# Optimization experiments

Hardware: AMD Instinct MI355X
Metric: run time of the kernel (lower is better)

## Reference

```python
import jax, jax.numpy as jnp
import numpy as np

N_NODES = 100000


def gcn_conv(x, W, b, edge_index, n_nodes):
    # PyG GCNConv (default args): add self-loops, symmetric normalization,
    # linear transform first, then normalized scatter-add aggregation, then bias.
    h = x @ W  # [N, out]
    loop = jnp.arange(n_nodes, dtype=edge_index.dtype)
    row = jnp.concatenate([edge_index[0], loop])  # sources
    col = jnp.concatenate([edge_index[1], loop])  # targets
    deg = jax.ops.segment_sum(jnp.ones_like(col, dtype=h.dtype), col, num_segments=n_nodes)
    dinv = jnp.where(deg > 0, jax.lax.rsqrt(deg), 0.0)
    norm = dinv[row] * dinv[col]  # [E']
    msg = h[row] * norm[:, None]  # gather + scale
    out = jax.ops.segment_sum(msg, col, num_segments=n_nodes)  # scatter-add
    return out + b


def setup_inputs() -> dict:
    key = jax.random.key(0)
    k1, k2, k3, k4 = jax.random.split(key, 4)
    N, E, F, H, C = N_NODES, 3200000, 128, 16, 8
    x = jax.random.normal(k1, (N, F), dtype=jnp.float32)
    edge_index = jax.random.randint(k2, (2, E), 0, N, dtype=jnp.int64)
    W1 = jax.random.normal(k3, (F, H), dtype=jnp.float32) / np.sqrt(F)
    b1 = jnp.zeros((H,), dtype=jnp.float32)
    W2 = jax.random.normal(k4, (H, C), dtype=jnp.float32) / np.sqrt(H)
    b2 = jnp.zeros((C,), dtype=jnp.float32)
    return {"x": x, "edge_index": edge_index, "W1": W1, "b1": b1, "W2": W2, "b2": b2}


def reference(x, edge_index, W1, b1, W2, b2):
    n = x.shape[0]
    h = jax.nn.relu(gcn_conv(x, W1, b1, edge_index, n))
    # F.dropout(training=self.training) is identity in eval mode
    out = gcn_conv(h, W2, b2, edge_index, n)
    return jax.nn.log_softmax(out, axis=1)
```

## Files before the change

### kernel.cpp

```cpp
#include <hip/hip_runtime.h>
#include <hip/hip_fp16.h>

#define F_IN 128
#define H1   16
#define C2   8
#define BSHIFT 7
#define BNODES 128
#define MAXBUCK 1024
#define NBLK 512
#define CAP  6144
#define MAXPER ((CAP + NBLK - 1) / NBLK)

__global__ __launch_bounds__(512) void binScatter2_kernel(
        const int* __restrict__ ei, int E, int chunk, int nbuck,
        int* __restrict__ bbcScan, int* __restrict__ stage) {
    __shared__ int h[MAXBUCK];
    __shared__ int sc[512];
    int t = threadIdx.x;
    int blk = blockIdx.x;
    int base = blk * chunk;
    int csize = max(0, min(chunk, E - base));
    int blkBase = base;

    for (int i = t; i < MAXBUCK; i += 512) h[i] = 0;
    __syncthreads();

    const int* colp = ei + E + base;
    const int* rowp = ei + base;
    bool al4 = ((E & 3) == 0) && ((base & 3) == 0) && ((csize & 3) == 0);

    if (al4) {
        const int4* cv = reinterpret_cast<const int4*>(colp);
        int nv = csize >> 2;
        for (int i = t; i < nv; i += 512) {
            int4 c4 = cv[i];
            atomicAdd(&h[c4.x >> BSHIFT], 1);
            atomicAdd(&h[c4.y >> BSHIFT], 1);
            atomicAdd(&h[c4.z >> BSHIFT], 1);
            atomicAdd(&h[c4.w >> BSHIFT], 1);
        }
    } else {
        for (int i = t; i < csize; i += 512) atomicAdd(&h[colp[i] >> BSHIFT], 1);
    }
    __syncthreads();

    int e0 = h[2 * t], e1 = h[2 * t + 1];
    int psum = e0 + e1;
    sc[t] = psum;
    __syncthreads();
    for (int off = 1; off < 512; off <<= 1) {
        int tmp = (t >= off) ? sc[t - off] : 0;
        __syncthreads();
        sc[t] += tmp;
        __syncthreads();
    }
    int excl = sc[t] - psum;
    h[2 * t] = blkBase + excl;
    h[2 * t + 1] = blkBase + excl + e0;
    __syncthreads();

    for (int b = t; b < nbuck; b += 512)
        bbcScan[blk * nbuck + b] = h[b];
    __syncthreads();

    if (al4) {
        const int4* cv = reinterpret_cast<const int4*>(colp);
        const int4* rv = reinterpret_cast<const int4*>(rowp);
        int nv = csize >> 2;
        for (int i = t; i < nv; i += 512) {
            int4 c4 = cv[i];
            int4 r4 = rv[i];
            int p0 = atomicAdd(&h[c4.x >> BSHIFT], 1);
            stage[p0] = (r4.x << BSHIFT) | (c4.x & (BNODES - 1));
            int p1 = atomicAdd(&h[c4.y >> BSHIFT], 1);
            stage[p1] = (r4.y << BSHIFT) | (c4.y & (BNODES - 1));
            int p2 = atomicAdd(&h[c4.z >> BSHIFT], 1);
            stage[p2] = (r4.z << BSHIFT) | (c4.z & (BNODES - 1));
            int p3 = atomicAdd(&h[c4.w >> BSHIFT], 1);
            stage[p3] = (r4.w << BSHIFT) | (c4.w & (BNODES - 1));
        }
    } else {
        for (int i = t; i < csize; i += 512) {
            int r = rowp[i];
            int c = colp[i];
            int p = atomicAdd(&h[c >> BSHIFT], 1);
            stage[p] = (r << BSHIFT) | (c & (BNODES - 1));
        }
    }
}

__global__ __launch_bounds__(NBLK) void sortCSR_kernel(
        const int* __restrict__ stage, const int* __restrict__ bbcScan,
        int E, int nbuck, int chunk, int* __restrict__ srt,
        int* __restrict__ nodePtr, float* __restrict__ dinv, int N) {
    __shared__ int ldsRec[CAP];
    __shared__ int pref[NBLK];
    __shared__ int cnt[BNODES];
    __shared__ int cur[BNODES];
    int b = blockIdx.x;
    int t = threadIdx.x;

    int winS = t * chunk;
    int runS = bbcScan[t * nbuck + b];
    int runE = (b + 1 < nbuck) ? bbcScan[t * nbuck + b + 1] : min((t + 1) * chunk, E);
    runE = min(runE, E);
    winS = min(winS, E);
    int sz = runE - runS;

    pref[t] = runS - winS;
    __syncthreads();
    for (int off = NBLK / 2; off > 0; off >>= 1) {
        if (t < off) pref[t] += pref[t + off];
        __syncthreads();
    }
    int bucketStart = pref[0];
    __syncthreads();

    pref[t] = sz;
    __syncthreads();
    for (int off = 1; off < NBLK; off <<= 1) {
        int tmp = (t >= off) ? pref[t - off] : 0;
        __syncthreads();
        pref[t] += tmp;
        __syncthreads();
    }
    int myOff = pref[t] - sz;
    int T = pref[NBLK - 1];

    if (t < BNODES) cnt[t] = 0;
    __syncthreads();

    bool fit = (T <= CAP);
    int rk[MAXPER];
    if (fit) {
        for (int i = 0; i < sz; ++i) ldsRec[myOff + i] = stage[runS + i];
        __syncthreads();
#pragma unroll
        for (int kk = 0; kk < MAXPER; ++kk) {
            int k = t + kk * NBLK;
            if (k < T) rk[kk] = atomicAdd(&cnt[ldsRec[k] & (BNODES - 1)], 1);
        }
    } else {
        for (int i = runS; i < runE; ++i)
            atomicAdd(&cnt[stage[i] & (BNODES - 1)], 1);
    }
    __syncthreads();

    if (t < BNODES) cur[t] = cnt[t];
    __syncthreads();
    for (int off = 1; off < BNODES; off <<= 1) {
        int tmp = 0;
        if (t < BNODES && t >= off) tmp = cur[t - off];
        __syncthreads();
        if (t < BNODES) cur[t] += tmp;
        __syncthreads();
    }
    if (t < BNODES) {
        int excl = cur[t] - cnt[t];
        int v = b * BNODES + t;
        if (v < N) {
            nodePtr[v] = bucketStart + excl;
            dinv[v] = rsqrtf((float)cnt[t] + 1.0f);
        }
        cur[t] = excl;
    }
    if (b == nbuck - 1 && t == 0) nodePtr[N] = E;
    __syncthreads();

    if (fit) {
#pragma unroll
        for (int kk = 0; kk < MAXPER; ++kk) {
            int k = t + kk * NBLK;
            if (k < T) {
                int rec = ldsRec[k];
                srt[bucketStart + cur[rec & (BNODES - 1)] + rk[kk]] = rec >> BSHIFT;
            }
        }
    } else {
        for (int i = runS; i < runE; ++i) {
            int rec = stage[i];
            int p = atomicAdd(&cur[rec & (BNODES - 1)], 1);
            srt[bucketStart + p] = rec >> BSHIFT;
        }
    }
}

__global__ void gemm1_kernel(const float* __restrict__ x, const float* __restrict__ W1,
                             const float* __restrict__ dinv, __half* __restrict__ h1h, int N) {
    __shared__ float sW[F_IN * H1];
    for (int i = threadIdx.x; i < F_IN * H1; i += blockDim.x) sW[i] = W1[i];
    __syncthreads();
    int v = blockIdx.x * blockDim.x + threadIdx.x;
    if (v >= N) return;
    float acc[H1];
#pragma unroll
    for (int j = 0; j < H1; ++j) acc[j] = 0.0f;
    const float4* xr = reinterpret_cast<const float4*>(x + (size_t)v * F_IN);
#pragma unroll 8
    for (int k4 = 0; k4 < F_IN / 4; ++k4) {
        float4 xv = xr[k4];
        const float* w = &sW[k4 * 4 * H1];
#pragma unroll
        for (int j = 0; j < H1; ++j) acc[j] += xv.x * w[j];
#pragma unroll
        for (int j = 0; j < H1; ++j) acc[j] += xv.y * w[H1 + j];
#pragma unroll
        for (int j = 0; j < H1; ++j) acc[j] += xv.z * w[2 * H1 + j];
#pragma unroll
        for (int j = 0; j < H1; ++j) acc[j] += xv.w * w[3 * H1 + j];
    }
    float di = dinv[v];
    alignas(16) __half2 hp[8];
#pragma unroll
    for (int q = 0; q < 8; ++q)
        hp[q] = __floats2half2_rn(acc[2 * q] * di, acc[2 * q + 1] * di);
    float4* ho = reinterpret_cast<float4*>(h1h + (size_t)v * H1);
    ho[0] = *reinterpret_cast<float4*>(&hp[0]);
    ho[1] = *reinterpret_cast<float4*>(&hp[4]);
}

#define AGG1_TB 512
__global__ __launch_bounds__(AGG1_TB) void agg1_kernel(
        const int* __restrict__ srt, const int* __restrict__ nodePtr,
        const __half* __restrict__ h1h, const float* __restrict__ dinv,
        const float* __restrict__ b1, const float* __restrict__ W2,
        __half* __restrict__ h2h, int N) {
    __shared__ float hrelu[BNODES][H1 + 1];
    __shared__ float sW[H1 * C2];
    __shared__ float sb[H1];
    for (int i = threadIdx.x; i < H1 * C2; i += AGG1_TB) sW[i] = W2[i];
    for (int i = threadIdx.x; i < H1; i += AGG1_TB) sb[i] = b1[i];
    __syncthreads();

    int base = blockIdx.x * BNODES;
    int vi = threadIdx.x >> 2;
    int ep = (threadIdx.x >> 1) & 1;
    int q  = threadIdx.x & 1;
    int v  = base + vi;

    if (v < N) {
        int p  = nodePtr[v];
        int pe = nodePtr[v + 1];
        float a0[8], a1[8];
#pragma unroll
        for (int k = 0; k < 8; ++k) { a0[k] = 0.f; a1[k] = 0.f; }
        int e = p + ep;
        for (; e + 2 < pe; e += 4) {
            int r0 = srt[e];
            int r1 = srt[e + 2];
            float4 p0 = *reinterpret_cast<const float4*>(h1h + (size_t)r0 * H1 + q * 8);
            float4 p1 = *reinterpret_cast<const float4*>(h1h + (size_t)r1 * H1 + q * 8);
            const __half2* h0 = reinterpret_cast<const __half2*>(&p0);
            const __half2* h1_ = reinterpret_cast<const __half2*>(&p1);
#pragma unroll
            for (int k = 0; k < 4; ++k) {
                float2 f0 = __half22float2(h0[k]);
                float2 f1 = __half22float2(h1_[k]);
                a0[2 * k] += f0.x; a0[2 * k + 1] += f0.y;
                a1[2 * k] += f1.x; a1[2 * k + 1] += f1.y;
            }
        }
        for (; e < pe; e += 2) {
            int r0 = srt[e];
            float4 p0 = *reinterpret_cast<const float4*>(h1h + (size_t)r0 * H1 + q * 8);
            const __half2* h0 = reinterpret_cast<const __half2*>(&p0);
#pragma unroll
            for (int k = 0; k < 4; ++k) {
                float2 f0 = __half22float2(h0[k]);
                a0[2 * k] += f0.x; a0[2 * k + 1] += f0.y;
            }
        }
#pragma unroll
        for (int k = 0; k < 8; ++k) a0[k] += a1[k];
#pragma unroll
        for (int k = 0; k < 8; ++k) a0[k] += __shfl_xor(a0[k], 2);

        if (ep == 0) {
            float4 ps = *reinterpret_cast<const float4*>(h1h + (size_t)v * H1 + q * 8);
            const __half2* hs = reinterpret_cast<const __half2*>(&ps);
            float di = dinv[v];
#pragma unroll
            for (int k = 0; k < 4; ++k) {
                float2 fs = __half22float2(hs[k]);
                int j0 = q * 8 + 2 * k, j1 = j0 + 1;
                hrelu[vi][j0] = fmaxf(di * (a0[2 * k] + fs.x) + sb[j0], 0.0f);
                hrelu[vi][j1] = fmaxf(di * (a0[2 * k + 1] + fs.y) + sb[j1], 0.0f);
            }
        }
    }
    __syncthreads();

    int j = threadIdx.x & 7;
    for (int vi2 = threadIdx.x >> 3; vi2 < BNODES; vi2 += (AGG1_TB >> 3)) {
        int v2 = base + vi2;
        if (v2 < N) {
            float dot = 0.0f;
#pragma unroll
            for (int k = 0; k < H1; ++k) dot += hrelu[vi2][k] * sW[k * C2 + j];
            h2h[(size_t)v2 * C2 + j] = __float2half(dot * dinv[v2]);
        }
    }
}

#define AGG2_TB 256
__global__ __launch_bounds__(AGG2_TB) void agg2_kernel(
        const int* __restrict__ srt, const int* __restrict__ nodePtr,
        const __half* __restrict__ h2h, const float* __restrict__ dinv,
        const float* __restrict__ b2, float* __restrict__ out, int N) {
    int vi  = threadIdx.x >> 1;
    int par = threadIdx.x & 1;
    int v = blockIdx.x * (AGG2_TB / 2) + vi;
    if (v >= N) return;
    int p  = nodePtr[v];
    int pe = nodePtr[v + 1];
    float a0[8], a1[8];
#pragma unroll
    for (int k = 0; k < 8; ++k) { a0[k] = 0.f; a1[k] = 0.f; }
    int e = p + par;
    for (; e + 2 < pe; e += 4) {
        int r0 = srt[e];
        int r1 = srt[e + 2];
        float4 p0 = *reinterpret_cast<const float4*>(h2h + (size_t)r0 * C2);
        float4 p1 = *reinterpret_cast<const float4*>(h2h + (size_t)r1 * C2);
        const __half2* h0 = reinterpret_cast<const __half2*>(&p0);
        const __half2* h1_ = reinterpret_cast<const __half2*>(&p1);
#pragma unroll
        for (int k = 0; k < 4; ++k) {
            float2 f0 = __half22float2(h0[k]);
            float2 f1 = __half22float2(h1_[k]);
            a0[2 * k] += f0.x; a0[2 * k + 1] += f0.y;
            a1[2 * k] += f1.x; a1[2 * k + 1] += f1.y;
        }
    }
    for (; e < pe; e += 2) {
        int r0 = srt[e];
        float4 p0 = *reinterpret_cast<const float4*>(h2h + (size_t)r0 * C2);
        const __half2* h0 = reinterpret_cast<const __half2*>(&p0);
#pragma unroll
        for (int k = 0; k < 4; ++k) {
            float2 f0 = __half22float2(h0[k]);
            a0[2 * k] += f0.x; a0[2 * k + 1] += f0.y;
        }
    }
#pragma unroll
    for (int k = 0; k < 8; ++k) a0[k] += a1[k];
#pragma unroll
    for (int k = 0; k < 8; ++k) a0[k] += __shfl_xor(a0[k], 1);
    if (par) return;

    float4 ps = *reinterpret_cast<const float4*>(h2h + (size_t)v * C2);
    const __half2* hs = reinterpret_cast<const __half2*>(&ps);
    float di = dinv[v];
    float z[C2];
#pragma unroll
    for (int k = 0; k < 4; ++k) {
        float2 fs = __half22float2(hs[k]);
        z[2 * k]     = di * (a0[2 * k] + fs.x) + b2[2 * k];
        z[2 * k + 1] = di * (a0[2 * k + 1] + fs.y) + b2[2 * k + 1];
    }
    float m = z[0];
#pragma unroll
    for (int j = 1; j < C2; ++j) m = fmaxf(m, z[j]);
    float s = 0.0f;
#pragma unroll
    for (int j = 0; j < C2; ++j) s += __expf(z[j] - m);
    float lse = m + logf(s);
    float4* o = reinterpret_cast<float4*>(out + (size_t)v * C2);
    o[0] = make_float4(z[0] - lse, z[1] - lse, z[2] - lse, z[3] - lse);
    o[1] = make_float4(z[4] - lse, z[5] - lse, z[6] - lse, z[7] - lse);
}

extern "C" void kernel_launch(void* const* d_in, const int* in_sizes, int n_in,
                              void* d_out, int out_size, void* d_ws, size_t ws_size,
                              hipStream_t stream) {
    const float* x  = (const float*)d_in[0];
    const int*   ei = (const int*)d_in[1];
    const float* W1 = (const float*)d_in[2];
    const float* b1 = (const float*)d_in[3];
    const float* W2 = (const float*)d_in[4];
    const float* b2 = (const float*)d_in[5];
    float* out = (float*)d_out;

    const int N = in_sizes[0] / F_IN;
    const int E = in_sizes[1] / 2;
    const int nbuck = (N + BNODES - 1) >> BSHIFT;
    const int M = NBLK * nbuck;
    int chunk = (E + NBLK - 1) / NBLK;
    chunk = (chunk + 3) & ~3;

    int*    stage   = (int*)d_ws;
    int*    srt     = stage + E;
    int*    bbcScan = srt + E;
    int*    nodePtr = bbcScan + M;
    float*  dinv    = (float*)(nodePtr + N + 8);
    __half* h1h     = (__half*)(dinv + N);
    __half* h2h     = h1h + (size_t)16 * N;

    const int TB = 256;

    binScatter2_kernel<<<NBLK, 512, 0, stream>>>(ei, E, chunk, nbuck, bbcScan, stage);
    sortCSR_kernel<<<nbuck, NBLK, 0, stream>>>(stage, bbcScan, E, nbuck, chunk, srt, nodePtr, dinv, N);
    gemm1_kernel<<<(N + TB - 1) / TB, TB, 0, stream>>>(x, W1, dinv, h1h, N);
    agg1_kernel<<<nbuck, AGG1_TB, 0, stream>>>(srt, nodePtr, h1h, dinv, b1, W2, h2h, N);
    agg2_kernel<<<(N + (AGG2_TB / 2) - 1) / (AGG2_TB / 2), AGG2_TB, 0, stream>>>(srt, nodePtr, h2h, dinv, b2, out, N);
}
```

Measured before the change: 135.9 us.

## Halve sort block count and fuse rank atomics into staged-record copy loop

Result: faster. 126.7 us (-6.7%).

```diff
diff --git a/kernel.cpp b/kernel.cpp
--- a/kernel.cpp
+++ b/kernel.cpp
@@ -7,9 +7,8 @@
 #define BSHIFT 7
 #define BNODES 128
 #define MAXBUCK 1024
-#define NBLK 512
+#define NBLK 256
 #define CAP  6144
-#define MAXPER ((CAP + NBLK - 1) / NBLK)
 
 __global__ __launch_bounds__(512) void binScatter2_kernel(
         const int* __restrict__ ei, int E, int chunk, int nbuck,
@@ -94,17 +93,17 @@
         int E, int nbuck, int chunk, int* __restrict__ srt,
         int* __restrict__ nodePtr, float* __restrict__ dinv, int N) {
     __shared__ int ldsRec[CAP];
+    __shared__ unsigned char ranks[CAP];
     __shared__ int pref[NBLK];
     __shared__ int cnt[BNODES];
     __shared__ int cur[BNODES];
     int b = blockIdx.x;
     int t = threadIdx.x;
 
-    int winS = t * chunk;
-    int runS = bbcScan[t * nbuck + b];
+    int winS = min(t * chunk, E);
+    int runS = min(bbcScan[t * nbuck + b], E);
     int runE = (b + 1 < nbuck) ? bbcScan[t * nbuck + b + 1] : min((t + 1) * chunk, E);
     runE = min(runE, E);
-    winS = min(winS, E);
     int sz = runE - runS;
 
     pref[t] = runS - winS;
@@ -131,14 +130,11 @@
     __syncthreads();
 
     bool fit = (T <= CAP);
-    int rk[MAXPER];
     if (fit) {
-        for (int i = 0; i < sz; ++i) ldsRec[myOff + i] = stage[runS + i];
-        __syncthreads();
-#pragma unroll
-        for (int kk = 0; kk < MAXPER; ++kk) {
-            int k = t + kk * NBLK;
-            if (k < T) rk[kk] = atomicAdd(&cnt[ldsRec[k] & (BNODES - 1)], 1);
+        for (int i = 0; i < sz; ++i) {
+            int rec = stage[runS + i];
+            ldsRec[myOff + i] = rec;
+            ranks[myOff + i] = (unsigned char)atomicAdd(&cnt[rec & (BNODES - 1)], 1);
         }
     } else {
         for (int i = runS; i < runE; ++i)
@@ -162,25 +158,21 @@
             nodePtr[v] = bucketStart + excl;
             dinv[v] = rsqrtf((float)cnt[t] + 1.0f);
         }
-        cur[t] = excl;
+        cur[t] = bucketStart + excl;
     }
     if (b == nbuck - 1 && t == 0) nodePtr[N] = E;
     __syncthreads();
 
     if (fit) {
-#pragma unroll
-        for (int kk = 0; kk < MAXPER; ++kk) {
-            int k = t + kk * NBLK;
-            if (k < T) {
-                int rec = ldsRec[k];
-                srt[bucketStart + cur[rec & (BNODES - 1)] + rk[kk]] = rec >> BSHIFT;
-            }
+        for (int i = 0; i < sz; ++i) {
+            int rec = ldsRec[myOff + i];
+            srt[cur[rec & (BNODES - 1)] + (int)ranks[myOff + i]] = rec >> BSHIFT;
         }
     } else {
         for (int i = runS; i < runE; ++i) {
             int rec = stage[i];
             int p = atomicAdd(&cur[rec & (BNODES - 1)], 1);
-            srt[bucketStart + p] = rec >> BSHIFT;
+            srt[p] = rec >> BSHIFT;
         }
     }
 }
```
